# Performance work log

Hardware: AMD Instinct MI355X
Metric: run time of the kernel (lower is better)

The kernel has to match this reference:

```python
import jax, jax.numpy as jnp
import numpy as np

D_MODEL = 1024
NUM_HEADS = 16
DEPTH = D_MODEL // NUM_HEADS
B, S = 8, 1024


def setup_inputs() -> dict:
    key = jax.random.key(0)
    ks = jax.random.split(key, 12)
    sc = 1.0 / np.sqrt(D_MODEL)
    inp = {
        "q": jax.random.normal(ks[0], (B, S, D_MODEL), jnp.float32),
        "k": jax.random.normal(ks[1], (B, S, D_MODEL), jnp.float32),
        "v": jax.random.normal(ks[2], (B, S, D_MODEL), jnp.float32),
        "mask": jax.random.randint(ks[3], (B, 1, 1, S - 1), 0, 2, jnp.int32),
        "wq_w": jax.random.normal(ks[4], (D_MODEL, D_MODEL), jnp.float32) * sc,
        "wq_b": jnp.zeros((D_MODEL,), jnp.float32),
        "wk_w": jax.random.normal(ks[5], (D_MODEL, D_MODEL), jnp.float32) * sc,
        "wk_b": jnp.zeros((D_MODEL,), jnp.float32),
        "wv_w": jax.random.normal(ks[6], (D_MODEL, D_MODEL), jnp.float32) * sc,
        "wv_b": jnp.zeros((D_MODEL,), jnp.float32),
        "dense_w": jax.random.normal(ks[7], (D_MODEL, D_MODEL), jnp.float32) * sc,
        "dense_b": jnp.zeros((D_MODEL,), jnp.float32),
    }
    return inp


def _split_heads(x):
    # [B,S,D] -> [B,H,S,depth]
    b, s, _ = x.shape
    return x.reshape(b, s, NUM_HEADS, DEPTH).transpose(0, 2, 1, 3)


def reference(q, k, v, mask, wq_w, wq_b, wk_w, wk_b, wv_w, wv_b, dense_w, dense_b):
    qh = _split_heads(q @ wq_w.T + wq_b)
    kh = _split_heads(k @ wk_w.T + wk_b)
    vh = _split_heads(v @ wv_w.T + wv_b)
    scale = 1.0 / (np.sqrt(DEPTH) + 1e-8)
    # scores: [B,H,S,S]
    scores = jnp.einsum("bhqd,bhkd->bhqk", qh, kh) * scale
    # prepend an always-valid column: mask [B,1,1,S-1] -> [B,1,1,S]
    mask_cat = jnp.concatenate(
        [jnp.ones(mask.shape[:-1] + (1,), mask.dtype), mask], axis=-1
    )
    scores = jnp.where(mask_cat == 0, -jnp.inf, scores)
    attn = jax.nn.softmax(scores, axis=-1)
    out = jnp.einsum("bhqk,bhkd->bhqd", attn, vh)
    out = out.transpose(0, 2, 1, 3).reshape(q.shape[0], -1, D_MODEL)
    output = out @ dense_w.T + dense_b
    return output, attn
```

## Files before the change

### kernel.cpp

```cpp
#include <hip/hip_runtime.h>
#include <hip/hip_fp16.h>

#define D_MODEL 1024
#define NHEADS  16
#define DEPTH   64
#define BATCH   8
#define SEQ     1024

typedef __attribute__((ext_vector_type(4))) float    floatx4;
typedef __attribute__((ext_vector_type(8))) _Float16 half8;
typedef __attribute__((ext_vector_type(4))) _Float16 half4;

static __device__ __forceinline__ void async16(const void* g, void* l) {
    auto gp = reinterpret_cast<const __attribute__((address_space(1))) unsigned int*>(
        reinterpret_cast<uintptr_t>(g));
    auto lp = reinterpret_cast<__attribute__((address_space(3))) unsigned int*>(
        reinterpret_cast<uintptr_t>(l));
    __builtin_amdgcn_global_load_lds(gp, lp, 16, 0, 0);
}

__global__ void cvt_f32_f16(const float* __restrict__ src, _Float16* __restrict__ dst, int n4) {
    int i = blockIdx.x * 256 + threadIdx.x;
    if (i >= n4) return;
    const float4 f = ((const float4*)src)[i];
    half4 o = { (_Float16)f.x, (_Float16)f.y, (_Float16)f.z, (_Float16)f.w };
    ((half4*)dst)[i] = o;
}

template <int OUT_HALF>
__global__ __launch_bounds__(256, 2) void gemm_bt(
    const _Float16* __restrict__ A, const _Float16* __restrict__ Bw,
    const float* __restrict__ bias, void* __restrict__ Cout,
    int M, int N, int K)
{
    __shared__ _Float16 sA[128 * 64];
    __shared__ _Float16 sB[128 * 64];

    const int tid  = threadIdx.x;
    const int wave = tid >> 6, lane = tid & 63;
    const int quad = lane >> 4, l16 = lane & 15;
    const int bm = blockIdx.x, bn = blockIdx.y;
    const int wy = wave & 1, wx = wave >> 1;

    floatx4 acc[4][4] = {};

    const int srow = wave * 8 + (lane >> 3);
    const int kpp  = lane & 7;

    for (int k0 = 0; k0 < K; k0 += 64) {
        __syncthreads();
#pragma unroll
        for (int r = 0; r < 4; ++r) {
            const int row = srow + r * 32;
            const int kpl = kpp ^ (row & 7);
            const _Float16* gA = A  + (size_t)(bm * 128 + row) * K + k0 + kpl * 8;
            const _Float16* gB = Bw + (size_t)(bn * 128 + row) * K + k0 + kpl * 8;
            async16(gA, sA + (r * 256 + wave * 64) * 8);
            async16(gB, sB + (r * 256 + wave * 64) * 8);
        }
        __syncthreads();
#pragma unroll
        for (int ks = 0; ks < 2; ++ks) {
            half8 af[4], bf[4];
#pragma unroll
            for (int i = 0; i < 4; ++i) {
                const int rowA = wy * 64 + i * 16 + l16;
                af[i] = *(const half8*)(sA + rowA * 64 + (((ks * 4 + quad) ^ (rowA & 7)) * 8));
                const int rowB = wx * 64 + i * 16 + l16;
                bf[i] = *(const half8*)(sB + rowB * 64 + (((ks * 4 + quad) ^ (rowB & 7)) * 8));
            }
#pragma unroll
            for (int i = 0; i < 4; ++i)
#pragma unroll
                for (int j = 0; j < 4; ++j)
                    acc[i][j] = __builtin_amdgcn_mfma_f32_16x16x32_f16(af[i], bf[j], acc[i][j], 0, 0, 0);
        }
    }

#pragma unroll
    for (int i = 0; i < 4; ++i) {
        const int row0 = bm * 128 + wy * 64 + i * 16 + quad * 4;
#pragma unroll
        for (int j = 0; j < 4; ++j) {
            const int col = bn * 128 + wx * 64 + j * 16 + l16;
            const float bv = bias[col];
#pragma unroll
            for (int r = 0; r < 4; ++r) {
                const float vv = acc[i][j][r] + bv;
                if (OUT_HALF) ((_Float16*)Cout)[(size_t)(row0 + r) * N + col] = (_Float16)vv;
                else          ((float*)Cout)   [(size_t)(row0 + r) * N + col] = vv;
            }
        }
    }
}

__global__ __launch_bounds__(256) void transpose_v(const _Float16* __restrict__ vp,
                                                   _Float16* __restrict__ vt) {
    __shared__ _Float16 t[64][72];
    const int tid = threadIdx.x;
    const int s0 = blockIdx.x * 64;
    const int bh = blockIdx.y;
    const int b = bh >> 4, h = bh & 15;
    {
        const int si = tid >> 2, dj = (tid & 3) * 16;
        const _Float16* src = vp + (size_t)(b * SEQ + s0 + si) * D_MODEL + h * 64 + dj;
        *(half8*)&t[si][dj]     = *(const half8*)src;
        *(half8*)&t[si][dj + 8] = *(const half8*)(src + 8);
    }
    __syncthreads();
    {
        const int d = tid >> 2, sj = (tid & 3) * 16;
        _Float16* dst = vt + (size_t)(bh * 64 + d) * SEQ + s0 + sj;
        half8 v0, v1;
#pragma unroll
        for (int j = 0; j < 8; ++j) { v0[j] = t[sj + j][d]; v1[j] = t[sj + 8 + j][d]; }
        *(half8*)dst       = v0;
        *(half8*)(dst + 8) = v1;
    }
}

__global__ __launch_bounds__(256, 4) void attn_fused(
    const _Float16* __restrict__ qp, const _Float16* __restrict__ kp,
    const _Float16* __restrict__ vt, const int* __restrict__ mask,
    float* __restrict__ attn, _Float16* __restrict__ ctx)
{
    __shared__ _Float16 pb[16 * 1024];
    __shared__ float maddend[1024];
    __shared__ float red0[4][16];
    __shared__ float red1[4][16];

    const int tid  = threadIdx.x;
    const int wave = tid >> 6, lane = tid & 63;
    const int quad = lane >> 4, l16 = lane & 15;
    const int q0 = blockIdx.x * 16;
    const int bh = blockIdx.y;
    const int b = bh >> 4, h = bh & 15;
    const float scale = 1.0f / (sqrtf(64.0f) + 1e-8f);
    const float NEGINF = -__builtin_inff();

    {
        const int c = tid * 4;
        const int* mrow = mask + b * (SEQ - 1);
        float4 a4;
        a4.x = (c == 0) ? 0.f : (mrow[c - 1] ? 0.f : NEGINF);
        a4.y = mrow[c + 0] ? 0.f : NEGINF;
        a4.z = mrow[c + 1] ? 0.f : NEGINF;
        a4.w = mrow[c + 2] ? 0.f : NEGINF;
        *(float4*)&maddend[c] = a4;
    }

    const half8 qf0 = *(const half8*)(qp + (size_t)(b * SEQ + q0 + l16) * D_MODEL + h * 64 + quad * 8);
    const half8 qf1 = *(const half8*)(qp + (size_t)(b * SEQ + q0 + l16) * D_MODEL + h * 64 + 32 + quad * 8);
    __syncthreads();

    float s[16][4];
#pragma unroll
    for (int t = 0; t < 16; ++t) {
        const int ct = wave * 16 + t;
        const half8 kf0 = *(const half8*)(kp + (size_t)(b * SEQ + ct * 16 + l16) * D_MODEL + h * 64 + quad * 8);
        const half8 kf1 = *(const half8*)(kp + (size_t)(b * SEQ + ct * 16 + l16) * D_MODEL + h * 64 + 32 + quad * 8);
        floatx4 a = {0.f, 0.f, 0.f, 0.f};
        a = __builtin_amdgcn_mfma_f32_16x16x32_f16(kf0, qf0, a, 0, 0, 0);
        a = __builtin_amdgcn_mfma_f32_16x16x32_f16(kf1, qf1, a, 0, 0, 0);
        const float4 ma = *(const float4*)&maddend[ct * 16 + quad * 4];
        s[t][0] = a[0] * scale + ma.x;
        s[t][1] = a[1] * scale + ma.y;
        s[t][2] = a[2] * scale + ma.z;
        s[t][3] = a[3] * scale + ma.w;
    }

    float pm = NEGINF;
#pragma unroll
    for (int t = 0; t < 16; ++t)
#pragma unroll
        for (int r = 0; r < 4; ++r) pm = fmaxf(pm, s[t][r]);
    pm = fmaxf(pm, __shfl_xor(pm, 16, 64));
    pm = fmaxf(pm, __shfl_xor(pm, 32, 64));
    if (lane < 16) red0[wave][lane] = pm;
    __syncthreads();
    const float m = fmaxf(fmaxf(red0[0][l16], red0[1][l16]),
                          fmaxf(red0[2][l16], red0[3][l16]));

    float ps = 0.f;
#pragma unroll
    for (int t = 0; t < 16; ++t)
#pragma unroll
        for (int r = 0; r < 4; ++r) { s[t][r] = __expf(s[t][r] - m); ps += s[t][r]; }
    ps += __shfl_xor(ps, 16, 64);
    ps += __shfl_xor(ps, 32, 64);
    if (lane < 16) red1[wave][lane] = ps;
    __syncthreads();
    const float inv = 1.0f / (red1[0][l16] + red1[1][l16] + red1[2][l16] + red1[3][l16]);

#pragma unroll
    for (int t = 0; t < 16; ++t) {
        const int ct = wave * 16 + t;
        half4 hp = { (_Float16)(s[t][0] * inv), (_Float16)(s[t][1] * inv),
                     (_Float16)(s[t][2] * inv), (_Float16)(s[t][3] * inv) };
        const int chunk = (ct * 4 + quad) ^ ((l16 & 7) << 1);
        *(half4*)((char*)pb + l16 * 2048 + (chunk << 3)) = hp;
    }
    __syncthreads();

    floatx4 oacc = {0.f, 0.f, 0.f, 0.f};
    const _Float16* vrow = vt + (size_t)(bh * 64 + wave * 16 + l16) * SEQ;
#pragma unroll
    for (int it = 0; it < 32; ++it) {
        const int k0 = it * 32;
        const int mchunk = ((k0 >> 3) + quad) ^ (l16 & 7);
        const half8 af = *(const half8*)((char*)pb + l16 * 2048 + (mchunk << 4));
        const half8 vf = *(const half8*)(vrow + k0 + quad * 8);
        oacc = __builtin_amdgcn_mfma_f32_16x16x32_f16(af, vf, oacc, 0, 0, 0);
        if (it & 1) {
            const int w = it >> 1;
            const int r = wave * 4 + (w >> 2);
            const int g = w & 3;
            const int c8 = g * 64 + lane;
            const int pc = c8 ^ ((r & 7) << 1);
            const half4 hv = *(const half4*)((char*)pb + r * 2048 + (pc << 3));
            float4 f;
            f.x = (float)hv[0]; f.y = (float)hv[1]; f.z = (float)hv[2]; f.w = (float)hv[3];
            *(float4*)(attn + ((size_t)bh * SEQ + q0 + r) * SEQ + c8 * 4) = f;
        }
    }
#pragma unroll
    for (int r = 0; r < 4; ++r)
        ctx[(size_t)(b * SEQ + q0 + quad * 4 + r) * D_MODEL + h * 64 + wave * 16 + l16] = (_Float16)oacc[r];
}

extern "C" void kernel_launch(void* const* d_in, const int* in_sizes, int n_in,
                              void* d_out, int out_size, void* d_ws, size_t ws_size,
                              hipStream_t stream) {
    (void)in_sizes; (void)n_in; (void)out_size; (void)ws_size;
    const float* q    = (const float*)d_in[0];
    const float* k    = (const float*)d_in[1];
    const float* v    = (const float*)d_in[2];
    const int*   mask = (const int*)d_in[3];
    const float* wq_w = (const float*)d_in[4];
    const float* wq_b = (const float*)d_in[5];
    const float* wk_w = (const float*)d_in[6];
    const float* wk_b = (const float*)d_in[7];
    const float* wv_w = (const float*)d_in[8];
    const float* wv_b = (const float*)d_in[9];
    const float* dw   = (const float*)d_in[10];
    const float* db   = (const float*)d_in[11];

    float* outp  = (float*)d_out;
    float* attnp = outp + (size_t)BATCH * SEQ * D_MODEL;

    const size_t NQKV = (size_t)BATCH * SEQ * D_MODEL;
    const size_t NW   = (size_t)D_MODEL * D_MODEL;
    _Float16* tmpA  = (_Float16*)d_ws;
    _Float16* tmpW  = tmpA + NQKV;
    _Float16* qproj = tmpW + NW;
    _Float16* kproj = qproj + NQKV;
    _Float16* vproj = kproj + NQKV;

    const int M = BATCH * SEQ;
    const dim3 gg(M / 128, D_MODEL / 128);

    cvt_f32_f16<<<NQKV / 4 / 256, 256, 0, stream>>>(q, tmpA, (int)(NQKV / 4));
    cvt_f32_f16<<<NW / 4 / 256,  256, 0, stream>>>(wq_w, tmpW, (int)(NW / 4));
    gemm_bt<1><<<gg, 256, 0, stream>>>(tmpA, tmpW, wq_b, qproj, M, D_MODEL, D_MODEL);
    cvt_f32_f16<<<NQKV / 4 / 256, 256, 0, stream>>>(k, tmpA, (int)(NQKV / 4));
    cvt_f32_f16<<<NW / 4 / 256,  256, 0, stream>>>(wk_w, tmpW, (int)(NW / 4));
    gemm_bt<1><<<gg, 256, 0, stream>>>(tmpA, tmpW, wk_b, kproj, M, D_MODEL, D_MODEL);
    cvt_f32_f16<<<NQKV / 4 / 256, 256, 0, stream>>>(v, tmpA, (int)(NQKV / 4));
    cvt_f32_f16<<<NW / 4 / 256,  256, 0, stream>>>(wv_w, tmpW, (int)(NW / 4));
    gemm_bt<1><<<gg, 256, 0, stream>>>(tmpA, tmpW, wv_b, vproj, M, D_MODEL, D_MODEL);
    transpose_v<<<dim3(SEQ / 64, BATCH * NHEADS), 256, 0, stream>>>(vproj, tmpA);
    attn_fused<<<dim3(SEQ / 16, BATCH * NHEADS), 256, 0, stream>>>(qproj, kproj, tmpA, mask, attnp, vproj);
    cvt_f32_f16<<<NW / 4 / 256, 256, 0, stream>>>(dw, tmpW, (int)(NW / 4));
    gemm_bt<0><<<gg, 256, 0, stream>>>(vproj, tmpW, db, outp, M, D_MODEL, D_MODEL);
}
```

Baseline: 950.8 us.

## Batch QKV conversions and projections into single launches using attn buffer as scratch

Replaces six separate f32-to-f16 conversion kernels with one combined conversion kernel, and runs the three Q/K/V projection GEMMs as a single launch with a z-dimension selecting input, weight and bias. Converted inputs are staged in the attention output buffer before it is overwritten, and launch bounds are raised to request three blocks per CU. The intent is to cut launch overhead and tail effects and to give the GPU a larger grid to fill. The risk is register pressure from the higher occupancy target and the ordering dependency on reusing the attn output region as scratch.

```diff
diff --git a/kernel.cpp b/kernel.cpp
--- a/kernel.cpp
+++ b/kernel.cpp
@@ -27,10 +27,33 @@
     ((half4*)dst)[i] = o;
 }
 
+__global__ __launch_bounds__(256) void cvt_all(
+    const float* __restrict__ q, const float* __restrict__ k, const float* __restrict__ v,
+    const float* __restrict__ w0, const float* __restrict__ w1, const float* __restrict__ w2,
+    _Float16* __restrict__ dst)
+{
+    const int i = blockIdx.x * 256 + threadIdx.x;
+    const int IN4 = 1 << 21;
+    const int W4  = 1 << 18;
+    const float* src; int off;
+    if (i < 3 * IN4) {
+        const int which = i >> 21; off = i & (IN4 - 1);
+        src = which == 0 ? q : (which == 1 ? k : v);
+    } else {
+        const int j = i - 3 * IN4;
+        const int which = j >> 18; off = j & (W4 - 1);
+        src = which == 0 ? w0 : (which == 1 ? w1 : w2);
+    }
+    const float4 f = ((const float4*)src)[off];
+    half4 o = { (_Float16)f.x, (_Float16)f.y, (_Float16)f.z, (_Float16)f.w };
+    ((half4*)dst)[i] = o;
+}
+
 template <int OUT_HALF>
-__global__ __launch_bounds__(256, 2) void gemm_bt(
+__global__ __launch_bounds__(256, 3) void gemm_bt(
     const _Float16* __restrict__ A, const _Float16* __restrict__ Bw,
-    const float* __restrict__ bias, void* __restrict__ Cout,
+    const float* __restrict__ bias0, const float* __restrict__ bias1,
+    const float* __restrict__ bias2, void* __restrict__ Cout,
     int M, int N, int K)
 {
     __shared__ _Float16 sA[128 * 64];
@@ -39,8 +62,12 @@
     const int tid  = threadIdx.x;
     const int wave = tid >> 6, lane = tid & 63;
     const int quad = lane >> 4, l16 = lane & 15;
-    const int bm = blockIdx.x, bn = blockIdx.y;
+    const int bm = blockIdx.x, bn = blockIdx.y, bz = blockIdx.z;
     const int wy = wave & 1, wx = wave >> 1;
+
+    const float* bias = bz == 0 ? bias0 : (bz == 1 ? bias1 : bias2);
+    const _Float16* Abase = A  + (size_t)bz * M * K + (size_t)(bm * 128) * K;
+    const _Float16* Bbase = Bw + (size_t)bz * N * K + (size_t)(bn * 128) * K;
 
     floatx4 acc[4][4] = {};
 
@@ -53,10 +80,8 @@
         for (int r = 0; r < 4; ++r) {
             const int row = srow + r * 32;
             const int kpl = kpp ^ (row & 7);
-            const _Float16* gA = A  + (size_t)(bm * 128 + row) * K + k0 + kpl * 8;
-            const _Float16* gB = Bw + (size_t)(bn * 128 + row) * K + k0 + kpl * 8;
-            async16(gA, sA + (r * 256 + wave * 64) * 8);
-            async16(gB, sB + (r * 256 + wave * 64) * 8);
+            async16(Abase + (size_t)row * K + k0 + kpl * 8, sA + (r * 256 + wave * 64) * 8);
+            async16(Bbase + (size_t)row * K + k0 + kpl * 8, sB + (r * 256 + wave * 64) * 8);
         }
         __syncthreads();
 #pragma unroll
@@ -77,6 +102,7 @@
         }
     }
 
+    const size_t czoff = (size_t)bz * M * N;
 #pragma unroll
     for (int i = 0; i < 4; ++i) {
         const int row0 = bm * 128 + wy * 64 + i * 16 + quad * 4;
@@ -87,8 +113,8 @@
 #pragma unroll
             for (int r = 0; r < 4; ++r) {
                 const float vv = acc[i][j][r] + bv;
-                if (OUT_HALF) ((_Float16*)Cout)[(size_t)(row0 + r) * N + col] = (_Float16)vv;
-                else          ((float*)Cout)   [(size_t)(row0 + r) * N + col] = vv;
+                if (OUT_HALF) ((_Float16*)Cout)[czoff + (size_t)(row0 + r) * N + col] = (_Float16)vv;
+                else          ((float*)Cout)   [czoff + (size_t)(row0 + r) * N + col] = vv;
             }
         }
     }
@@ -250,26 +276,25 @@
 
     const size_t NQKV = (size_t)BATCH * SEQ * D_MODEL;
     const size_t NW   = (size_t)D_MODEL * D_MODEL;
-    _Float16* tmpA  = (_Float16*)d_ws;
-    _Float16* tmpW  = tmpA + NQKV;
-    _Float16* qproj = tmpW + NW;
+    const int    M    = BATCH * SEQ;
+
+    _Float16* qproj = (_Float16*)d_ws;
     _Float16* kproj = qproj + NQKV;
     _Float16* vproj = kproj + NQKV;
-
-    const int M = BATCH * SEQ;
-    const dim3 gg(M / 128, D_MODEL / 128);
-
-    cvt_f32_f16<<<NQKV / 4 / 256, 256, 0, stream>>>(q, tmpA, (int)(NQKV / 4));
-    cvt_f32_f16<<<NW / 4 / 256,  256, 0, stream>>>(wq_w, tmpW, (int)(NW / 4));
-    gemm_bt<1><<<gg, 256, 0, stream>>>(tmpA, tmpW, wq_b, qproj, M, D_MODEL, D_MODEL);
-    cvt_f32_f16<<<NQKV / 4 / 256, 256, 0, stream>>>(k, tmpA, (int)(NQKV / 4));
-    cvt_f32_f16<<<NW / 4 / 256,  256, 0, stream>>>(wk_w, tmpW, (int)(NW / 4));
-    gemm_bt<1><<<gg, 256, 0, stream>>>(tmpA, tmpW, wk_b, kproj, M, D_MODEL, D_MODEL);
-    cvt_f32_f16<<<NQKV / 4 / 256, 256, 0, stream>>>(v, tmpA, (int)(NQKV / 4));
-    cvt_f32_f16<<<NW / 4 / 256,  256, 0, stream>>>(wv_w, tmpW, (int)(NW / 4));
-    gemm_bt<1><<<gg, 256, 0, stream>>>(tmpA, tmpW, wv_b, vproj, M, D_MODEL, D_MODEL);
-    transpose_v<<<dim3(SEQ / 64, BATCH * NHEADS), 256, 0, stream>>>(vproj, tmpA);
-    attn_fused<<<dim3(SEQ / 16, BATCH * NHEADS), 256, 0, stream>>>(qproj, kproj, tmpA, mask, attnp, vproj);
-    cvt_f32_f16<<<NW / 4 / 256, 256, 0, stream>>>(dw, tmpW, (int)(NW / 4));
-    gemm_bt<0><<<gg, 256, 0, stream>>>(vproj, tmpW, db, outp, M, D_MODEL, D_MODEL);
-}
+    _Float16* vtb   = vproj + NQKV;
+    _Float16* sc     = (_Float16*)attnp;
+    _Float16* w3f16  = sc + 3 * NQKV;
+    _Float16* ctx    = vproj;
+    _Float16* dw16   = vtb;
+
+    const int CVT_BLOCKS = (3 * (1 << 21) + 3 * (1 << 18)) / 256;
+    cvt_all<<<CVT_BLOCKS, 256, 0, stream>>>(q, k, v, wq_w, wk_w, wv_w, sc);
+    gemm_bt<1><<<dim3(M / 128, D_MODEL / 128, 3), 256, 0, stream>>>(
+        sc, w3f16, wq_b, wk_b, wv_b, qproj, M, D_MODEL, D_MODEL);
+    transpose_v<<<dim3(SEQ / 64, BATCH * NHEADS), 256, 0, stream>>>(vproj, vtb);
+    attn_fused<<<dim3(SEQ / 16, BATCH * NHEADS), 256, 0, stream>>>(
+        qproj, kproj, vtb, mask, attnp, ctx);
+    cvt_f32_f16<<<(int)(NW / 4 / 256), 256, 0, stream>>>(dw, dw16, (int)(NW / 4));
+    gemm_bt<0><<<dim3(M / 128, D_MODEL / 128, 1), 256, 0, stream>>>(
+        ctx, dw16, db, db, db, outp, M, D_MODEL, D_MODEL);
+}
```

Measured after the change: 925.6 us. 2.7% less time.
